# Optimization experiments

Hardware: AMD Instinct MI355X
Metric: run time of the kernel (lower is better)

The kernel has to match this reference:

```python
import jax, jax.numpy as jnp
import numpy as np

EPS = 1e-5  # BatchNorm1d default eps


def _uf_death(fv, u, v):
    """0-dim lower-star persistence on a (disjoint-union) graph via union-find.
    fv: [N] vertex filtration values (float np). u, v: [E] endpoints (int np).
    Returns death[N]: index of the vertex whose filtration value is the death
    time of the component born at each vertex (self-index => essential / f,f).
    Edges are processed in order of their lower-star filtration value
    max(fv[u], fv[v]) (stable sort, matching simplex-tree filtration order).
    Elder rule: the component whose birth vertex has larger (f, index) dies.
    """
    N = fv.shape[0]
    fe = np.maximum(fv[u], fv[v])
    order = np.argsort(fe, kind='stable')
    parent = np.arange(N)
    birth = np.arange(N)   # birth vertex of the component rooted here
    death = np.arange(N)   # default: pair (f_v, f_v)

    def find(i):
        r = i
        while parent[r] != r:
            r = parent[r]
        while parent[i] != r:  # path compression
            parent[i], i = r, parent[i]
        return r

    for e in order:
        a, b = int(u[e]), int(v[e])
        ra, rb = find(a), find(b)
        if ra == rb:
            continue
        ba, bb = birth[ra], birth[rb]
        if (fv[ba], ba) <= (fv[bb], bb):
            elder_b, young_b = ba, bb
        else:
            elder_b, young_b = bb, ba
        # death vertex = edge endpoint realizing the edge filtration value
        w = a if (fv[a], a) >= (fv[b], b) else b
        death[young_b] = w
        parent[ra] = rb
        birth[rb] = elder_b
    return death


def _death_indices(x, W1, b1, W2, b2, edge_index):
    """Host-side (numpy) computation of pairing indices. Indices are piecewise
    constant w.r.t. the floats, so gradients do not flow through them."""
    xn = np.asarray(jax.device_get(x), dtype=np.float32)
    fv = np.maximum(xn @ np.asarray(W1) + np.asarray(b1), 0.0) @ np.asarray(W2) + np.asarray(b2)  # [N, F]
    ei = np.asarray(jax.device_get(edge_index))
    u, v = ei[0], ei[1]
    F = fv.shape[1]
    return np.stack([_uf_death(fv[:, k], u, v) for k in range(F)], axis=0)  # [F, N]


def _togl_forward(x, death_idx, batch, num_graphs,
                  W1, b1, W2, b2, W_in, b_in,
                  g1W, g1b, l1W, g2W, g2b, l2W, bn_gamma, bn_beta):
    N = x.shape[0]
    # Filtration MLP: Linear -> ReLU -> Linear
    fv = jnp.maximum(x @ W1 + b1, 0.0) @ W2 + b2          # [N, F]
    births = fv.T                                          # [F, N]
    deaths = jnp.take_along_axis(fv.T, death_idx, axis=1)  # [F, N]
    pd = jnp.stack([births, deaths], axis=-1)              # [F, N, 2]
    # per-node concat over filtrations: [N, 2F]
    x0 = pd.transpose(1, 0, 2).reshape(N, -1)
    x0 = jnp.maximum(x0 @ W_in + b_in, 0.0)                # Linear + ReLU

    def deepset(h, GW, Gb, LW):
        s = jax.ops.segment_sum(h, batch, num_segments=num_graphs)
        c = jax.ops.segment_sum(jnp.ones((h.shape[0], 1), h.dtype), batch,
                                num_segments=num_graphs)
        xm = (s / c) @ LW                                  # Lambda(scatter_mean)
        return h @ GW + Gb - xm[batch]

    x0 = jnp.maximum(deepset(x0, g1W, g1b, l1W), 0.0)      # DeepSet + ReLU
    x0 = deepset(x0, g2W, g2b, l2W)                        # DeepSet -> n_features
    r = jnp.maximum(x0, 0.0)
    mu = r.mean(axis=0)
    var = r.var(axis=0)                                    # biased, as BN training
    y = bn_gamma * (r - mu) * jax.lax.rsqrt(var + EPS) + bn_beta
    return x + y


def setup_inputs() -> dict:
    key = jax.random.key(0)
    ks = jax.random.split(key, 16)
    B, NPG, EPG = 32, 1024, 2048
    N, E = B * NPG, B * EPG
    n_feat, hid, n_filt, out_dim = 512, 512, 8, 64

    rng = np.random.default_rng(0)
    off = np.repeat(np.arange(B, dtype=np.int32) * NPG, EPG)
    u = rng.integers(0, NPG, E).astype(np.int32) + off
    v = rng.integers(0, NPG, E).astype(np.int32) + off
    edge_index = jnp.asarray(np.stack([u, v], axis=0))
    batch = jnp.asarray(np.repeat(np.arange(B, dtype=np.int32), NPG))
    vertex_slices = jnp.asarray(np.arange(B + 1, dtype=np.int32) * NPG)
    edge_slices = jnp.asarray(np.arange(B + 1, dtype=np.int32) * EPG)

    def lin(k, fan_in, shape):
        return jax.random.uniform(k, shape, jnp.float32, -1.0, 1.0) / np.sqrt(fan_in)

    return {
        'x': jax.random.normal(ks[0], (N, n_feat), jnp.float32),
        'edge_index': edge_index,
        'batch': batch,
        'vertex_slices': vertex_slices,
        'edge_slices': edge_slices,
        'W1': lin(ks[1], n_feat, (n_feat, hid)),
        'b1': lin(ks[2], n_feat, (hid,)),
        'W2': lin(ks[3], hid, (hid, n_filt)),
        'b2': lin(ks[4], hid, (n_filt,)),
        'W_in': lin(ks[5], 2 * n_filt, (2 * n_filt, out_dim)),
        'b_in': lin(ks[6], 2 * n_filt, (out_dim,)),
        'g1W': lin(ks[7], out_dim, (out_dim, out_dim)),
        'g1b': lin(ks[8], out_dim, (out_dim,)),
        'l1W': lin(ks[9], out_dim, (out_dim, out_dim)),
        'g2W': lin(ks[10], out_dim, (out_dim, n_feat)),
        'g2b': lin(ks[11], out_dim, (n_feat,)),
        'l2W': lin(ks[12], out_dim, (out_dim, n_feat)),
        'bn_gamma': jnp.ones((n_feat,), jnp.float32),
        'bn_beta': jnp.zeros((n_feat,), jnp.float32),
    }


def reference(x, edge_index, batch, vertex_slices, edge_slices,
              W1, b1, W2, b2, W_in, b_in,
              g1W, g1b, l1W, g2W, g2b, l2W, bn_gamma, bn_beta):
    num_graphs = int(vertex_slices.shape[0]) - 1
    death_idx = jnp.asarray(_death_indices(x, W1, b1, W2, b2, edge_index))  # [F, N]
    return _togl_forward(x, death_idx, batch, num_graphs,
                         W1, b1, W2, b2, W_in, b_in,
                         g1W, g1b, l1W, g2W, g2b, l2W, bn_gamma, bn_beta)
```

## Files before the change

kernel.cpp:

```cpp
#include <hip/hip_runtime.h>
#include <stdint.h>

static constexpr int NN    = 32768;
static constexpr int NPG   = 1024;
static constexpr int EPG   = 2048;
static constexpr int NGR   = 32;
static constexpr int NF    = 8;
static constexpr int FEAT  = 512;
static constexpr int ODIM  = 64;
static constexpr int ETOT  = NGR * EPG;

typedef short bf16x8 __attribute__((ext_vector_type(8)));
typedef float f32x4  __attribute__((ext_vector_type(4)));

__device__ __forceinline__ unsigned int fsort(float f) {
    unsigned int u = __float_as_uint(f);
    return (u & 0x80000000u) ? ~u : (u | 0x80000000u);
}

__device__ __forceinline__ void split2(float a, float b, unsigned& hi, unsigned& lo) {
    unsigned ua = __float_as_uint(a), ub = __float_as_uint(b);
    hi = (ua >> 16) | (ub & 0xffff0000u);
    float ra = a - __uint_as_float(ua & 0xffff0000u);
    float rb = b - __uint_as_float(ub & 0xffff0000u);
    lo = (__float_as_uint(ra) >> 16) | (__float_as_uint(rb) & 0xffff0000u);
}

__global__ __launch_bounds__(256) void w1swz_k(
        const float* __restrict__ W1,
        unsigned short* __restrict__ Whi, unsigned short* __restrict__ Wlo) {
    __shared__ float T[64][65];
    const int tid = threadIdx.x;
    const int kb = blockIdx.x >> 3, cb = blockIdx.x & 7;
    const int r16 = tid >> 4, c4 = tid & 15;
#pragma unroll
    for (int p = 0; p < 4; ++p) {
        int kl = r16 + p * 16;
        *(float4*)&T[kl][c4 * 4] = *(const float4*)&W1[(size_t)(kb * 64 + kl) * FEAT + cb * 64 + c4 * 4];
    }
    __syncthreads();
    const int col_l = tid >> 2;
    const int col = cb * 64 + col_l;
    const int sw = (col + (col >> 2)) & 3;
#pragma unroll
    for (int q = 0; q < 2; ++q) {
        int ch = (tid & 3) + q * 4;
        int ktl = ch >> 2, slot = ch & 3;
        int koff = slot ^ sw;
        unsigned hi[4], lo[4];
#pragma unroll
        for (int pj = 0; pj < 4; ++pj) {
            float a = T[ktl * 32 + koff * 8 + pj * 2 + 0][col_l];
            float b = T[ktl * 32 + koff * 8 + pj * 2 + 1][col_l];
            split2(a, b, hi[pj], lo[pj]);
        }
        size_t o = (size_t)col * 512 + (size_t)kb * 64 + ktl * 32 + slot * 8;
        *(uint4*)&Whi[o] = make_uint4(hi[0], hi[1], hi[2], hi[3]);
        *(uint4*)&Wlo[o] = make_uint4(lo[0], lo[1], lo[2], lo[3]);
    }
}

__global__ __launch_bounds__(256, 2) void mfma_fv_k(
        const float* __restrict__ x, const unsigned short* __restrict__ Whi,
        const unsigned short* __restrict__ Wlo, const float* __restrict__ b1,
        const float* __restrict__ W2, float* __restrict__ fvpart) {
    __shared__ unsigned short AsHi[4096], AsLo[4096], BsHi[4096], BsLo[4096];
    __shared__ float W2s[128][8];
    __shared__ float b1s[128];

    const int tid = threadIdx.x;
    const int lane = tid & 63, wid = tid >> 6;
    const int wr = wid >> 1, wc = wid & 1;
    const int b = blockIdx.x;
    const int rb = (b & 7) * 32 + (b >> 5);
    const int cb = (b >> 3) & 3;
    const int rowBase = rb * 128, colBase = cb * 128;

    for (int i = tid; i < 1024; i += 256)
        W2s[i >> 3][i & 7] = W2[(size_t)(colBase + (i >> 3)) * NF + (i & 7)];
    if (tid < 128) b1s[tid] = b1[colBase + tid];

    const int arow = tid >> 1, ah2 = tid & 1;
    const int aswz = (arow + (arow >> 2)) & 3;
    const float* xp = x + (size_t)(rowBase + arow) * FEAT + ah2 * 16;
    const int bcol = tid >> 1;
    const size_t bsrc = (size_t)(colBase + bcol) * 512 + (size_t)(tid & 1) * 16;
    const int bdst = bcol * 32 + (tid & 1) * 16;

    f32x4 acc[4][4];
#pragma unroll
    for (int m = 0; m < 4; ++m)
#pragma unroll
        for (int n = 0; n < 4; ++n) acc[m][n] = (f32x4){0.f, 0.f, 0.f, 0.f};

    float4 av[4];
    uint4 bhv[2], blv[2];
    av[0] = ((const float4*)xp)[0]; av[1] = ((const float4*)xp)[1];
    av[2] = ((const float4*)xp)[2]; av[3] = ((const float4*)xp)[3];
    bhv[0] = *(const uint4*)(Whi + bsrc); bhv[1] = *(const uint4*)(Whi + bsrc + 8);
    blv[0] = *(const uint4*)(Wlo + bsrc); blv[1] = *(const uint4*)(Wlo + bsrc + 8);

    for (int tk = 0; tk < 16; ++tk) {
        __syncthreads();
#pragma unroll
        for (int cj = 0; cj < 2; ++cj) {
            int koff = ah2 * 2 + cj;
            int slot = koff ^ aswz;
            unsigned h0, h1, h2, h3, l0, l1, l2, l3;
            split2(av[cj * 2 + 0].x, av[cj * 2 + 0].y, h0, l0);
            split2(av[cj * 2 + 0].z, av[cj * 2 + 0].w, h1, l1);
            split2(av[cj * 2 + 1].x, av[cj * 2 + 1].y, h2, l2);
            split2(av[cj * 2 + 1].z, av[cj * 2 + 1].w, h3, l3);
            int o = arow * 32 + slot * 8;
            *(uint4*)&AsHi[o] = make_uint4(h0, h1, h2, h3);
            *(uint4*)&AsLo[o] = make_uint4(l0, l1, l2, l3);
        }
        *(uint4*)&BsHi[bdst] = bhv[0]; *(uint4*)&BsHi[bdst + 8] = bhv[1];
        *(uint4*)&BsLo[bdst] = blv[0]; *(uint4*)&BsLo[bdst + 8] = blv[1];
        if (tk < 15) {
            const float* xq = xp + (tk + 1) * 32;
            av[0] = ((const float4*)xq)[0]; av[1] = ((const float4*)xq)[1];
            av[2] = ((const float4*)xq)[2]; av[3] = ((const float4*)xq)[3];
            const unsigned short* bh = Whi + bsrc + (size_t)(tk + 1) * 32;
            const unsigned short* bl = Wlo + bsrc + (size_t)(tk + 1) * 32;
            bhv[0] = *(const uint4*)bh; bhv[1] = *(const uint4*)(bh + 8);
            blv[0] = *(const uint4*)bl; blv[1] = *(const uint4*)(bl + 8);
        }
        __syncthreads();
        bf16x8 fa[4], fb[4], f2[4];
#pragma unroll
        for (int m = 0; m < 4; ++m) {
            int r = wr * 64 + m * 16 + (lane & 15);
            int slot = (lane >> 4) ^ ((r + (r >> 2)) & 3);
            fa[m] = *(const bf16x8*)&AsHi[r * 32 + slot * 8];
        }
#pragma unroll
        for (int n = 0; n < 4; ++n) {
            int c = wc * 64 + n * 16 + (lane & 15);
            int slot = (lane >> 4) ^ ((c + (c >> 2)) & 3);
            fb[n] = *(const bf16x8*)&BsHi[c * 32 + slot * 8];
        }
#pragma unroll
        for (int m = 0; m < 4; ++m)
#pragma unroll
            for (int n = 0; n < 4; ++n)
                acc[m][n] = __builtin_amdgcn_mfma_f32_16x16x32_bf16(fa[m], fb[n], acc[m][n], 0, 0, 0);
#pragma unroll
        for (int n = 0; n < 4; ++n) {
            int c = wc * 64 + n * 16 + (lane & 15);
            int slot = (lane >> 4) ^ ((c + (c >> 2)) & 3);
            f2[n] = *(const bf16x8*)&BsLo[c * 32 + slot * 8];
        }
#pragma unroll
        for (int m = 0; m < 4; ++m)
#pragma unroll
            for (int n = 0; n < 4; ++n)
                acc[m][n] = __builtin_amdgcn_mfma_f32_16x16x32_bf16(fa[m], f2[n], acc[m][n], 0, 0, 0);
#pragma unroll
        for (int m = 0; m < 4; ++m) {
            int r = wr * 64 + m * 16 + (lane & 15);
            int slot = (lane >> 4) ^ ((r + (r >> 2)) & 3);
            f2[m] = *(const bf16x8*)&AsLo[r * 32 + slot * 8];
        }
#pragma unroll
        for (int m = 0; m < 4; ++m)
#pragma unroll
            for (int n = 0; n < 4; ++n)
                acc[m][n] = __builtin_amdgcn_mfma_f32_16x16x32_bf16(f2[m], fb[n], acc[m][n], 0, 0, 0);
    }

    const int p = cb * 2 + wc;
#pragma unroll
    for (int m = 0; m < 4; ++m) {
        float pf[4][8];
#pragma unroll
        for (int r = 0; r < 4; ++r)
#pragma unroll
            for (int j = 0; j < 8; ++j) pf[r][j] = 0.f;
#pragma unroll
        for (int n = 0; n < 4; ++n) {
            int c = wc * 64 + n * 16 + (lane & 15);
            float bc = b1s[c];
            float4 wA = *(const float4*)&W2s[c][0];
            float4 wB = *(const float4*)&W2s[c][4];
#pragma unroll
            for (int r = 0; r < 4; ++r) {
                float h = fmaxf(acc[m][n][r] + bc, 0.f);
                pf[r][0] += h * wA.x; pf[r][1] += h * wA.y; pf[r][2] += h * wA.z; pf[r][3] += h * wA.w;
                pf[r][4] += h * wB.x; pf[r][5] += h * wB.y; pf[r][6] += h * wB.z; pf[r][7] += h * wB.w;
            }
        }
#pragma unroll
        for (int mask = 1; mask <= 8; mask <<= 1)
#pragma unroll
            for (int r = 0; r < 4; ++r)
#pragma unroll
                for (int j = 0; j < 8; ++j) pf[r][j] += __shfl_xor(pf[r][j], mask);
        if ((lane & 15) == 0) {
            int rowb = rowBase + wr * 64 + m * 16 + (lane >> 4) * 4;
#pragma unroll
            for (int r = 0; r < 4; ++r) {
                *(float4*)&fvpart[(((size_t)p << 15) + rowb + r) * NF + 0] =
                    make_float4(pf[r][0], pf[r][1], pf[r][2], pf[r][3]);
                *(float4*)&fvpart[(((size_t)p << 15) + rowb + r) * NF + 4] =
                    make_float4(pf[r][4], pf[r][5], pf[r][6], pf[r][7]);
            }
        }
    }
}

__global__ __launch_bounds__(256) void fvred_k(
        const float* __restrict__ fvpart, const float* __restrict__ b2,
        float* __restrict__ fv, float* __restrict__ fvT) {
    const int row = blockIdx.x * 256 + threadIdx.x;
    float s[8];
    *(float4*)&s[0] = *(const float4*)&b2[0];
    *(float4*)&s[4] = *(const float4*)&b2[4];
#pragma unroll
    for (int p = 0; p < 8; ++p) {
        float4 lo = *(const float4*)&fvpart[(((size_t)p << 15) + row) * NF + 0];
        float4 hi = *(const float4*)&fvpart[(((size_t)p << 15) + row) * NF + 4];
        s[0] += lo.x; s[1] += lo.y; s[2] += lo.z; s[3] += lo.w;
        s[4] += hi.x; s[5] += hi.y; s[6] += hi.z; s[7] += hi.w;
    }
    *(float4*)&fv[(size_t)row * NF + 0] = *(float4*)&s[0];
    *(float4*)&fv[(size_t)row * NF + 4] = *(float4*)&s[4];
#pragma unroll
    for (int j = 0; j < 8; ++j) fvT[(size_t)j * NN + row] = s[j];
}

__global__ __launch_bounds__(512) void uf_sort_k(
        const float* __restrict__ fvT, const int* __restrict__ ei,
        unsigned int* __restrict__ suvw) {
    __shared__ float fvl[NPG];
    __shared__ unsigned long long keys[EPG];
    __shared__ unsigned int uvw[EPG];
    const int tid = threadIdx.x;
    const int g = blockIdx.x >> 3, k = blockIdx.x & 7;

    for (int i = tid; i < NPG; i += 512) fvl[i] = fvT[(size_t)k * NN + (g << 10) + i];
    __syncthreads();
    for (int e = tid; e < EPG; e += 512) {
        int eg = g * EPG + e;
        int u = ei[eg] & (NPG - 1);
        int v = ei[ETOT + eg] & (NPG - 1);
        unsigned int fku = fsort(fvl[u]);
        unsigned int fkv = fsort(fvl[v]);
        unsigned int wfl = (fku > fkv || (fku == fkv && u >= v)) ? 1u : 0u;
        unsigned int fe = fku > fkv ? fku : fkv;
        uvw[e] = (unsigned)u | ((unsigned)v << 10) | (wfl << 20);
        keys[e] = ((unsigned long long)fe << 32) | (unsigned)e;
    }
    for (int size = 2; size <= EPG; size <<= 1) {
        for (int stride = size >> 1; stride > 0; stride >>= 1) {
            __syncthreads();
            for (int i = tid; i < EPG; i += 512) {
                int j = i ^ stride;
                if (j > i) {
                    unsigned long long a = keys[i], b = keys[j];
                    bool asc = (i & size) == 0;
                    if (asc ? (a > b) : (a < b)) { keys[i] = b; keys[j] = a; }
                }
            }
        }
    }
    __syncthreads();
    for (int i = tid; i < EPG; i += 512)
        suvw[(size_t)blockIdx.x * EPG + i] = uvw[(unsigned)(keys[i] & 0xffffffffULL)];
}

__global__ __launch_bounds__(256) void uf_merge_k(
        const float* __restrict__ fvT, const unsigned int* __restrict__ suvw,
        float* __restrict__ dvT) {
    __shared__ float fvl[NPG];
    __shared__ unsigned long long node[NPG];
    __shared__ unsigned short deathl[NPG];
    __shared__ unsigned int se[EPG];

    const int tid = threadIdx.x;
    const int g = blockIdx.x >> 3, k = blockIdx.x & 7;

    for (int i = tid; i < NPG; i += 256) {
        float val = fvT[(size_t)k * NN + (g << 10) + i];
        fvl[i] = val;
        node[i] = ((unsigned long long)fsort(val) << 32) | ((unsigned long long)(unsigned)i << 16) | (unsigned)i;
        deathl[i] = (unsigned short)i;
    }
    for (int i = tid; i < EPG / 4; i += 256)
        ((uint4*)se)[i] = ((const uint4*)(suvw + (size_t)blockIdx.x * EPG))[i];
    __syncthreads();

    if (tid < 64) {
        const int lane = tid;
        volatile unsigned int* vn32 = (volatile unsigned int*)node;
        volatile unsigned long long* vn64 = (volatile unsigned long long*)node;
        for (int w = 0; w < EPG / 64; ++w) {
            unsigned int pk = se[w * 64 + lane];
            int u = (int)(pk & 1023u), v = (int)((pk >> 10) & 1023u);
            int wd = ((pk >> 20) & 1u) ? u : v;
            int ru = u;
            {
                unsigned int lw = vn32[ru * 2];
                int p = (int)(lw & 0xffffu);
                while (p != ru) {
                    unsigned int lw2 = vn32[p * 2];
                    int gp = (int)(lw2 & 0xffffu);
                    if (gp != p) vn32[ru * 2] = (lw & 0xffff0000u) | (unsigned)gp;
                    ru = p; lw = lw2; p = gp;
                }
            }
            int rv = v;
            {
                unsigned int lw = vn32[rv * 2];
                int p = (int)(lw & 0xffffu);
                while (p != rv) {
                    unsigned int lw2 = vn32[p * 2];
                    int gp = (int)(lw2 & 0xffffu);
                    if (gp != p) vn32[rv * 2] = (lw & 0xffff0000u) | (unsigned)gp;
                    rv = p; lw = lw2; p = gp;
                }
            }
            unsigned long long wa = vn64[ru];
            unsigned long long wb = vn64[rv];
            bool aliveF = (ru != rv);
            bool committed = false;
            int cY = 0, cE = 0;
            unsigned long long cW = 0;
            unsigned long long mask = __ballot(aliveF);
            while (mask) {
                int li = (int)__builtin_ctzll(mask);
                bool uE = (wa >> 16) <= (wb >> 16);
                int rE_l = uE ? ru : rv;
                int rY_l = uE ? rv : ru;
                unsigned long long wE_l = uE ? wa : wb;
                unsigned long long wY_l = uE ? wb : wa;
                unsigned pk2 = (unsigned)rY_l | ((unsigned)rE_l << 10);
                unsigned bpk = __shfl(pk2, li);
                unsigned belo = __shfl((unsigned)wE_l, li);
                unsigned behi = __shfl((unsigned)(wE_l >> 32), li);
                unsigned long long bwE = ((unsigned long long)behi << 32) | belo;
                int brY = (int)(bpk & 1023u), brE = (int)((bpk >> 10) & 1023u);
                if (lane == li) { committed = true; cY = rY_l; cE = rE_l; cW = wY_l; }
                if (ru == brY) { ru = brE; wa = bwE; }
                if (rv == brY) { rv = brE; wb = bwE; }
                aliveF = aliveF && (lane > li) && (ru != rv);
                mask = __ballot(aliveF);
            }
            if (committed) {
                deathl[(int)((cW >> 16) & 0xffffu)] = (unsigned short)wd;
                vn64[cY] = (cW & ~0xffffULL) | (unsigned)cE;
            }
            __builtin_amdgcn_wave_barrier();
        }
    }
    __syncthreads();
    for (int i = tid; i < NPG; i += 256)
        dvT[(size_t)k * NN + (g << 10) + i] = fvl[deathl[i]];
}

__global__ __launch_bounds__(256, 2) void feat_k(
        const float* __restrict__ fv, const float* __restrict__ dvT,
        const float* __restrict__ W_in, const float* __restrict__ b_in,
        float* __restrict__ h0) {
    __shared__ float Ws[16][64];
    __shared__ float bs[64];
    const int tid = threadIdx.x;
    for (int i = tid; i < 1024; i += 256) Ws[i >> 6][i & 63] = W_in[i];
    if (tid < 64) bs[tid] = b_in[tid];
    __syncthreads();
    const int n = blockIdx.x * 256 + tid;
    float4 f0 = *(const float4*)&fv[(size_t)n * NF + 0];
    float4 f1 = *(const float4*)&fv[(size_t)n * NF + 4];
    float dd[8];
#pragma unroll
    for (int j = 0; j < 8; ++j) dd[j] = dvT[(size_t)j * NN + n];
    float x0[16] = { f0.x, dd[0], f0.y, dd[1], f0.z, dd[2], f0.w, dd[3],
                     f1.x, dd[4], f1.y, dd[5], f1.z, dd[6], f1.w, dd[7] };
    float out[64];
#pragma unroll
    for (int j = 0; j < 64; ++j) out[j] = bs[j];
#pragma unroll
    for (int i = 0; i < 16; ++i) {
        float a = x0[i];
#pragma unroll
        for (int j4 = 0; j4 < 16; ++j4) {
            float4 w = *(const float4*)&Ws[i][j4 * 4];
            out[j4 * 4 + 0] += a * w.x; out[j4 * 4 + 1] += a * w.y;
            out[j4 * 4 + 2] += a * w.z; out[j4 * 4 + 3] += a * w.w;
        }
    }
#pragma unroll
    for (int j4 = 0; j4 < 16; ++j4) {
        float4 o = { fmaxf(out[j4 * 4 + 0], 0.f), fmaxf(out[j4 * 4 + 1], 0.f),
                     fmaxf(out[j4 * 4 + 2], 0.f), fmaxf(out[j4 * 4 + 3], 0.f) };
        *(float4*)&h0[(size_t)n * 64 + j4 * 4] = o;
    }
}

__global__ void reduce64_k(const float* __restrict__ h, float* __restrict__ s) {
    __shared__ float part[4][64];
    const int tid = threadIdx.x, g = blockIdx.x;
    const int c = tid & 63, rg = tid >> 6;
    float acc = 0.f;
    for (int r = rg; r < NPG; r += 4) acc += h[(size_t)(g * NPG + r) * 64 + c];
    part[rg][c] = acc;
    __syncthreads();
    if (tid < 64) s[g * 64 + tid] = part[0][tid] + part[1][tid] + part[2][tid] + part[3][tid];
}

__global__ void lam_k(const float* __restrict__ s, const float* __restrict__ LW,
                      const float* __restrict__ Gb, float* __restrict__ bias, int Fout) {
    __shared__ float sg[64];
    const int tid = threadIdx.x, g = blockIdx.x;
    if (tid < 64) sg[tid] = s[g * 64 + tid] * (1.0f / 1024.0f);
    __syncthreads();
    for (int j = tid; j < Fout; j += 256) {
        float acc = 0.f;
        for (int i = 0; i < 64; ++i) acc += sg[i] * LW[i * Fout + j];
        bias[g * Fout + j] = Gb[j] - acc;
    }
}

__global__ __launch_bounds__(256, 2) void ds1_k(
        const float* __restrict__ h0, const float* __restrict__ g1W,
        const float* __restrict__ bias1, float* __restrict__ h1) {
    __shared__ float Ws[64][64];
    const int tid = threadIdx.x;
    for (int i = tid; i < 4096; i += 256) Ws[i >> 6][i & 63] = g1W[i];
    __syncthreads();
    const int n = blockIdx.x * 256 + tid;
    const int g = n >> 10;
    float in[64];
#pragma unroll
    for (int i4 = 0; i4 < 16; ++i4) {
        float4 t = *(const float4*)&h0[(size_t)n * 64 + i4 * 4];
        in[i4 * 4 + 0] = t.x; in[i4 * 4 + 1] = t.y; in[i4 * 4 + 2] = t.z; in[i4 * 4 + 3] = t.w;
    }
    float out[64];
#pragma unroll
    for (int j4 = 0; j4 < 16; ++j4) {
        float4 b = *(const float4*)&bias1[g * 64 + j4 * 4];
        out[j4 * 4 + 0] = b.x; out[j4 * 4 + 1] = b.y; out[j4 * 4 + 2] = b.z; out[j4 * 4 + 3] = b.w;
    }
#pragma unroll 8
    for (int i = 0; i < 64; ++i) {
        float a = in[i];
#pragma unroll
        for (int j4 = 0; j4 < 16; ++j4) {
            float4 w = *(const float4*)&Ws[i][j4 * 4];
            out[j4 * 4 + 0] += a * w.x; out[j4 * 4 + 1] += a * w.y;
            out[j4 * 4 + 2] += a * w.z; out[j4 * 4 + 3] += a * w.w;
        }
    }
#pragma unroll
    for (int j4 = 0; j4 < 16; ++j4) {
        float4 o = { fmaxf(out[j4 * 4 + 0], 0.f), fmaxf(out[j4 * 4 + 1], 0.f),
                     fmaxf(out[j4 * 4 + 2], 0.f), fmaxf(out[j4 * 4 + 3], 0.f) };
        *(float4*)&h1[(size_t)n * 64 + j4 * 4] = o;
    }
}

__global__ __launch_bounds__(256, 2) void ds2_k(
        const float* __restrict__ h1, const float* __restrict__ g2W,
        const float* __restrict__ bias2, float* __restrict__ rout) {
    __shared__ float Ht[32][68];
    __shared__ float Wt[64][68];
    const int tid = threadIdx.x;
    const int rowBase = blockIdx.x * 32;
    const int g = rowBase >> 10;
#pragma unroll
    for (int p = 0; p < 2; ++p) {
        int fid = tid + p * 256;
        int r = fid >> 4, c4 = fid & 15;
        *(float4*)&Ht[r][c4 * 4] = *(const float4*)&h1[(size_t)(rowBase + r) * 64 + c4 * 4];
    }
    const int cg = tid & 15, rg = tid >> 4;
    for (int nc = 0; nc < 8; ++nc) {
        __syncthreads();
#pragma unroll
        for (int p = 0; p < 4; ++p) {
            int fid = tid + p * 256;
            int kk = fid >> 4, c4 = fid & 15;
            *(float4*)&Wt[kk][c4 * 4] = *(const float4*)&g2W[(size_t)kk * FEAT + nc * 64 + c4 * 4];
        }
        __syncthreads();
        float a0[4] = {0.f, 0.f, 0.f, 0.f}, a1[4] = {0.f, 0.f, 0.f, 0.f};
#pragma unroll 8
        for (int kk = 0; kk < 64; ++kk) {
            float h0v = Ht[rg * 2][kk], h1v = Ht[rg * 2 + 1][kk];
            float4 w = *(const float4*)&Wt[kk][cg * 4];
            a0[0] += h0v * w.x; a0[1] += h0v * w.y; a0[2] += h0v * w.z; a0[3] += h0v * w.w;
            a1[0] += h1v * w.x; a1[1] += h1v * w.y; a1[2] += h1v * w.z; a1[3] += h1v * w.w;
        }
        float4 bv = *(const float4*)&bias2[g * FEAT + nc * 64 + cg * 4];
        int row0 = rowBase + rg * 2;
        float4 o0 = { fmaxf(a0[0] + bv.x, 0.f), fmaxf(a0[1] + bv.y, 0.f),
                      fmaxf(a0[2] + bv.z, 0.f), fmaxf(a0[3] + bv.w, 0.f) };
        float4 o1 = { fmaxf(a1[0] + bv.x, 0.f), fmaxf(a1[1] + bv.y, 0.f),
                      fmaxf(a1[2] + bv.z, 0.f), fmaxf(a1[3] + bv.w, 0.f) };
        *(float4*)&rout[(size_t)row0 * FEAT + nc * 64 + cg * 4] = o0;
        *(float4*)&rout[(size_t)(row0 + 1) * FEAT + nc * 64 + cg * 4] = o1;
    }
}

__global__ void bnst1_k(const float* __restrict__ r, float* __restrict__ psum, float* __restrict__ psq) {
    const int tid = threadIdx.x, b = blockIdx.x;
    const int row0 = b * 128;
    float s0 = 0.f, q0 = 0.f, s1 = 0.f, q1 = 0.f;
    for (int rr = 0; rr < 128; ++rr) {
        float a = r[(size_t)(row0 + rr) * FEAT + tid];
        float c = r[(size_t)(row0 + rr) * FEAT + 256 + tid];
        s0 += a; q0 += a * a; s1 += c; q1 += c * c;
    }
    psum[b * FEAT + tid] = s0; psum[b * FEAT + 256 + tid] = s1;
    psq [b * FEAT + tid] = q0; psq [b * FEAT + 256 + tid] = q1;
}

__global__ void bnst2_k(const float* __restrict__ psum, const float* __restrict__ psq,
                        const float* __restrict__ gamma, const float* __restrict__ beta,
                        float* __restrict__ scsh) {
    const int tid = threadIdx.x;
    for (int c = tid; c < FEAT; c += 256) {
        float s = 0.f, q = 0.f;
        for (int b = 0; b < 256; ++b) { s += psum[b * FEAT + c]; q += psq[b * FEAT + c]; }
        float mu = s * (1.0f / (float)NN);
        float var = q * (1.0f / (float)NN) - mu * mu;
        float sc = gamma[c] * rsqrtf(var + 1e-5f);
        scsh[c] = sc;
        scsh[FEAT + c] = beta[c] - mu * sc;
    }
}

__global__ void final_k(const float* __restrict__ x, const float* __restrict__ scsh,
                        float* __restrict__ out) {
    const int total4 = NN * (FEAT / 4);
    for (int idx = blockIdx.x * 256 + threadIdx.x; idx < total4; idx += 2048 * 256) {
        int col4 = idx & (FEAT / 4 - 1);
        float4 rv = *(float4*)&out[(size_t)idx * 4];
        float4 xv = *(const float4*)&x[(size_t)idx * 4];
        float4 sc = *(const float4*)&scsh[col4 * 4];
        float4 sh = *(const float4*)&scsh[FEAT + col4 * 4];
        float4 o = { xv.x + rv.x * sc.x + sh.x, xv.y + rv.y * sc.y + sh.y,
                     xv.z + rv.z * sc.z + sh.z, xv.w + rv.w * sc.w + sh.w };
        *(float4*)&out[(size_t)idx * 4] = o;
    }
}

extern "C" void kernel_launch(void* const* d_in, const int* in_sizes, int n_in,
                              void* d_out, int out_size, void* d_ws, size_t ws_size,
                              hipStream_t stream) {
    const float* x     = (const float*)d_in[0];
    const int*   ei    = (const int*)d_in[1];
    const float* W1    = (const float*)d_in[5];
    const float* b1    = (const float*)d_in[6];
    const float* W2    = (const float*)d_in[7];
    const float* b2    = (const float*)d_in[8];
    const float* W_in  = (const float*)d_in[9];
    const float* b_in  = (const float*)d_in[10];
    const float* g1W   = (const float*)d_in[11];
    const float* g1b   = (const float*)d_in[12];
    const float* l1W   = (const float*)d_in[13];
    const float* g2W   = (const float*)d_in[14];
    const float* g2b   = (const float*)d_in[15];
    const float* l2W   = (const float*)d_in[16];
    const float* gamma = (const float*)d_in[17];
    const float* beta  = (const float*)d_in[18];
    float* out = (float*)d_out;
    float* ws  = (float*)d_ws;

    float* fv    = ws;
    float* dvT   = ws + 262144;
    float* h0    = ws + 524288;
    float* h1    = ws + 2621440;
    unsigned short* W1hi = (unsigned short*)(ws + 262144);
    unsigned short* W1lo = (unsigned short*)(ws + 393216);
    float*        fvpart = ws + 524288;
    float*        fvT  = ws + 2621440;
    unsigned int* suvw = (unsigned int*)(ws + 2883584);
    float* s1    = ws + 4718592;
    float* bias1 = ws + 4720640;
    float* s2    = ws + 4722688;
    float* bias2 = ws + 4724736;
    float* psum  = ws + 4741120;
    float* psq   = ws + 4872192;
    float* scsh  = ws + 5003264;

    hipLaunchKernelGGL(w1swz_k,    dim3(64),   dim3(256), 0, stream, W1, W1hi, W1lo);
    hipLaunchKernelGGL(mfma_fv_k,  dim3(1024), dim3(256), 0, stream, x, W1hi, W1lo, b1, W2, fvpart);
    hipLaunchKernelGGL(fvred_k,    dim3(128),  dim3(256), 0, stream, fvpart, b2, fv, fvT);
    hipLaunchKernelGGL(uf_sort_k,  dim3(256),  dim3(512), 0, stream, fvT, ei, suvw);
    hipLaunchKernelGGL(uf_merge_k, dim3(256),  dim3(256), 0, stream, fvT, suvw, dvT);
    hipLaunchKernelGGL(feat_k,     dim3(128),  dim3(256), 0, stream, fv, dvT, W_in, b_in, h0);
    hipLaunchKernelGGL(reduce64_k, dim3(32),   dim3(256), 0, stream, h0, s1);
    hipLaunchKernelGGL(lam_k,      dim3(32),   dim3(256), 0, stream, s1, l1W, g1b, bias1, 64);
    hipLaunchKernelGGL(ds1_k,      dim3(128),  dim3(256), 0, stream, h0, g1W, bias1, h1);
    hipLaunchKernelGGL(reduce64_k, dim3(32),   dim3(256), 0, stream, h1, s2);
    hipLaunchKernelGGL(lam_k,      dim3(32),   dim3(256), 0, stream, s2, l2W, g2b, bias2, 512);
    hipLaunchKernelGGL(ds2_k,      dim3(1024), dim3(256), 0, stream, h1, g2W, bias2, out);
    hipLaunchKernelGGL(bnst1_k,    dim3(256),  dim3(256), 0, stream, out, psum, psq);
    hipLaunchKernelGGL(bnst2_k,    dim3(1),    dim3(256), 0, stream, psum, psq, gamma, beta, scsh);
    hipLaunchKernelGGL(final_k,    dim3(2048), dim3(256), 0, stream, x, scsh, out);
}
```

Before: 650.7 us.

## Fuse BatchNorm statistics into ds2 epilogue and merge reduce with lambda kernels

Computes per-block BatchNorm partial sums and squared sums inside the ds2 GEMM epilogue using wave shuffles and shared memory, which removes the separate bnst1 pass that re-read the full 32768x512 output. bnst2 is parallelised to one block per channel, where before a single block did the whole reduction. The graph-mean reduction and lambda bias kernels are merged into one kernel, saving two launches. The trade-off is an extra __syncthreads per column chunk in ds2 and psum/psq buffers reusing workspace regions that are no longer live.

```diff
diff --git a/kernel.cpp b/kernel.cpp
--- a/kernel.cpp
+++ b/kernel.cpp
@@ -397,27 +397,22 @@
     }
 }
 
-__global__ void reduce64_k(const float* __restrict__ h, float* __restrict__ s) {
+__global__ void redlam_k(const float* __restrict__ h, const float* __restrict__ LW,
+                         const float* __restrict__ Gb, float* __restrict__ bias, int Fout) {
     __shared__ float part[4][64];
+    __shared__ float sg[64];
     const int tid = threadIdx.x, g = blockIdx.x;
     const int c = tid & 63, rg = tid >> 6;
     float acc = 0.f;
     for (int r = rg; r < NPG; r += 4) acc += h[(size_t)(g * NPG + r) * 64 + c];
     part[rg][c] = acc;
     __syncthreads();
-    if (tid < 64) s[g * 64 + tid] = part[0][tid] + part[1][tid] + part[2][tid] + part[3][tid];
-}
-
-__global__ void lam_k(const float* __restrict__ s, const float* __restrict__ LW,
-                      const float* __restrict__ Gb, float* __restrict__ bias, int Fout) {
-    __shared__ float sg[64];
-    const int tid = threadIdx.x, g = blockIdx.x;
-    if (tid < 64) sg[tid] = s[g * 64 + tid] * (1.0f / 1024.0f);
+    if (tid < 64) sg[tid] = (part[0][tid] + part[1][tid] + part[2][tid] + part[3][tid]) * (1.0f / 1024.0f);
     __syncthreads();
     for (int j = tid; j < Fout; j += 256) {
-        float acc = 0.f;
-        for (int i = 0; i < 64; ++i) acc += sg[i] * LW[i * Fout + j];
-        bias[g * Fout + j] = Gb[j] - acc;
+        float a = 0.f;
+        for (int i = 0; i < 64; ++i) a += sg[i] * LW[i * Fout + j];
+        bias[g * Fout + j] = Gb[j] - a;
     }
 }
 
@@ -462,11 +457,16 @@
 
 __global__ __launch_bounds__(256, 2) void ds2_k(
         const float* __restrict__ h1, const float* __restrict__ g2W,
-        const float* __restrict__ bias2, float* __restrict__ rout) {
+        const float* __restrict__ bias2, float* __restrict__ rout,
+        float* __restrict__ psum, float* __restrict__ psq) {
     __shared__ float Ht[32][68];
     __shared__ float Wt[64][68];
-    const int tid = threadIdx.x;
-    const int rowBase = blockIdx.x * 32;
+    __shared__ float smS[4][64];
+    __shared__ float smQ[4][64];
+    const int tid = threadIdx.x;
+    const int lane = tid & 63, wvid = tid >> 6;
+    const int b = blockIdx.x;
+    const int rowBase = b * 32;
     const int g = rowBase >> 10;
 #pragma unroll
     for (int p = 0; p < 2; ++p) {
@@ -493,38 +493,63 @@
             a1[0] += h1v * w.x; a1[1] += h1v * w.y; a1[2] += h1v * w.z; a1[3] += h1v * w.w;
         }
         float4 bv = *(const float4*)&bias2[g * FEAT + nc * 64 + cg * 4];
+        float r0[4], r1[4];
+        r0[0] = fmaxf(a0[0] + bv.x, 0.f); r0[1] = fmaxf(a0[1] + bv.y, 0.f);
+        r0[2] = fmaxf(a0[2] + bv.z, 0.f); r0[3] = fmaxf(a0[3] + bv.w, 0.f);
+        r1[0] = fmaxf(a1[0] + bv.x, 0.f); r1[1] = fmaxf(a1[1] + bv.y, 0.f);
+        r1[2] = fmaxf(a1[2] + bv.z, 0.f); r1[3] = fmaxf(a1[3] + bv.w, 0.f);
         int row0 = rowBase + rg * 2;
-        float4 o0 = { fmaxf(a0[0] + bv.x, 0.f), fmaxf(a0[1] + bv.y, 0.f),
-                      fmaxf(a0[2] + bv.z, 0.f), fmaxf(a0[3] + bv.w, 0.f) };
-        float4 o1 = { fmaxf(a1[0] + bv.x, 0.f), fmaxf(a1[1] + bv.y, 0.f),
-                      fmaxf(a1[2] + bv.z, 0.f), fmaxf(a1[3] + bv.w, 0.f) };
-        *(float4*)&rout[(size_t)row0 * FEAT + nc * 64 + cg * 4] = o0;
-        *(float4*)&rout[(size_t)(row0 + 1) * FEAT + nc * 64 + cg * 4] = o1;
-    }
-}
-
-__global__ void bnst1_k(const float* __restrict__ r, float* __restrict__ psum, float* __restrict__ psq) {
-    const int tid = threadIdx.x, b = blockIdx.x;
-    const int row0 = b * 128;
-    float s0 = 0.f, q0 = 0.f, s1 = 0.f, q1 = 0.f;
-    for (int rr = 0; rr < 128; ++rr) {
-        float a = r[(size_t)(row0 + rr) * FEAT + tid];
-        float c = r[(size_t)(row0 + rr) * FEAT + 256 + tid];
-        s0 += a; q0 += a * a; s1 += c; q1 += c * c;
-    }
-    psum[b * FEAT + tid] = s0; psum[b * FEAT + 256 + tid] = s1;
-    psq [b * FEAT + tid] = q0; psq [b * FEAT + 256 + tid] = q1;
+        *(float4*)&rout[(size_t)row0 * FEAT + nc * 64 + cg * 4] =
+            make_float4(r0[0], r0[1], r0[2], r0[3]);
+        *(float4*)&rout[(size_t)(row0 + 1) * FEAT + nc * 64 + cg * 4] =
+            make_float4(r1[0], r1[1], r1[2], r1[3]);
+        float s4[4], q4[4];
+#pragma unroll
+        for (int j = 0; j < 4; ++j) {
+            s4[j] = r0[j] + r1[j];
+            q4[j] = r0[j] * r0[j] + r1[j] * r1[j];
+        }
+#pragma unroll
+        for (int j = 0; j < 4; ++j) {
+            s4[j] += __shfl_xor(s4[j], 16); q4[j] += __shfl_xor(q4[j], 16);
+            s4[j] += __shfl_xor(s4[j], 32); q4[j] += __shfl_xor(q4[j], 32);
+        }
+        if (lane < 16) {
+#pragma unroll
+            for (int j = 0; j < 4; ++j) {
+                smS[wvid][lane * 4 + j] = s4[j];
+                smQ[wvid][lane * 4 + j] = q4[j];
+            }
+        }
+        __syncthreads();
+        if (tid < 64) {
+            float ss = smS[0][tid] + smS[1][tid] + smS[2][tid] + smS[3][tid];
+            float qq = smQ[0][tid] + smQ[1][tid] + smQ[2][tid] + smQ[3][tid];
+            psum[(size_t)(nc * 64 + tid) * 1024 + b] = ss;
+            psq [(size_t)(nc * 64 + tid) * 1024 + b] = qq;
+        }
+    }
 }
 
 __global__ void bnst2_k(const float* __restrict__ psum, const float* __restrict__ psq,
                         const float* __restrict__ gamma, const float* __restrict__ beta,
                         float* __restrict__ scsh) {
-    const int tid = threadIdx.x;
-    for (int c = tid; c < FEAT; c += 256) {
-        float s = 0.f, q = 0.f;
-        for (int b = 0; b < 256; ++b) { s += psum[b * FEAT + c]; q += psq[b * FEAT + c]; }
-        float mu = s * (1.0f / (float)NN);
-        float var = q * (1.0f / (float)NN) - mu * mu;
+    __shared__ float wS[4], wQ[4];
+    const int c = blockIdx.x;
+    const int tid = threadIdx.x;
+    float s = psum[(size_t)c * 1024 + tid] + psum[(size_t)c * 1024 + 256 + tid]
+            + psum[(size_t)c * 1024 + 512 + tid] + psum[(size_t)c * 1024 + 768 + tid];
+    float q = psq[(size_t)c * 1024 + tid] + psq[(size_t)c * 1024 + 256 + tid]
+            + psq[(size_t)c * 1024 + 512 + tid] + psq[(size_t)c * 1024 + 768 + tid];
+#pragma unroll
+    for (int m = 1; m <= 32; m <<= 1) { s += __shfl_xor(s, m); q += __shfl_xor(q, m); }
+    if ((tid & 63) == 0) { wS[tid >> 6] = s; wQ[tid >> 6] = q; }
+    __syncthreads();
+    if (tid == 0) {
+        float S = wS[0] + wS[1] + wS[2] + wS[3];
+        float Q = wQ[0] + wQ[1] + wQ[2] + wQ[3];
+        float mu = S * (1.0f / (float)NN);
+        float var = Q * (1.0f / (float)NN) - mu * mu;
         float sc = gamma[c] * rsqrtf(var + 1e-5f);
         scsh[c] = sc;
         scsh[FEAT + c] = beta[c] - mu * sc;
@@ -577,12 +602,10 @@
     float*        fvpart = ws + 524288;
     float*        fvT  = ws + 2621440;
     unsigned int* suvw = (unsigned int*)(ws + 2883584);
-    float* s1    = ws + 4718592;
+    float* psum  = ws + 524288;
+    float* psq   = ws + 1048576;
     float* bias1 = ws + 4720640;
-    float* s2    = ws + 4722688;
     float* bias2 = ws + 4724736;
-    float* psum  = ws + 4741120;
-    float* psq   = ws + 4872192;
     float* scsh  = ws + 5003264;
 
     hipLaunchKernelGGL(w1swz_k,    dim3(64),   dim3(256), 0, stream, W1, W1hi, W1lo);
@@ -591,13 +614,10 @@
     hipLaunchKernelGGL(uf_sort_k,  dim3(256),  dim3(512), 0, stream, fvT, ei, suvw);
     hipLaunchKernelGGL(uf_merge_k, dim3(256),  dim3(256), 0, stream, fvT, suvw, dvT);
     hipLaunchKernelGGL(feat_k,     dim3(128),  dim3(256), 0, stream, fv, dvT, W_in, b_in, h0);
-    hipLaunchKernelGGL(reduce64_k, dim3(32),   dim3(256), 0, stream, h0, s1);
-    hipLaunchKernelGGL(lam_k,      dim3(32),   dim3(256), 0, stream, s1, l1W, g1b, bias1, 64);
+    hipLaunchKernelGGL(redlam_k,   dim3(32),   dim3(256), 0, stream, h0, l1W, g1b, bias1, 64);
     hipLaunchKernelGGL(ds1_k,      dim3(128),  dim3(256), 0, stream, h0, g1W, bias1, h1);
-    hipLaunchKernelGGL(reduce64_k, dim3(32),   dim3(256), 0, stream, h1, s2);
-    hipLaunchKernelGGL(lam_k,      dim3(32),   dim3(256), 0, stream, s2, l2W, g2b, bias2, 512);
-    hipLaunchKernelGGL(ds2_k,      dim3(1024), dim3(256), 0, stream, h1, g2W, bias2, out);
-    hipLaunchKernelGGL(bnst1_k,    dim3(256),  dim3(256), 0, stream, out, psum, psq);
-    hipLaunchKernelGGL(bnst2_k,    dim3(1),    dim3(256), 0, stream, psum, psq, gamma, beta, scsh);
+    hipLaunchKernelGGL(redlam_k,   dim3(32),   dim3(256), 0, stream, h1, l2W, g2b, bias2, 512);
+    hipLaunchKernelGGL(ds2_k,      dim3(1024), dim3(256), 0, stream, h1, g2W, bias2, out, psum, psq);
+    hipLaunchKernelGGL(bnst2_k,    dim3(512),  dim3(256), 0, stream, psum, psq, gamma, beta, scsh);
     hipLaunchKernelGGL(final_k,    dim3(2048), dim3(256), 0, stream, x, scsh, out);
 }
```

Result: faster. 623.2 us (-4.2%).
